# Performance work log

Hardware: AMD Instinct MI355X
Metric: run time of the kernel (lower is better)

Reference implementation:

```python
import jax, jax.numpy as jnp
import numpy as np

NUM_EMBEDDINGS = 1024
EMBEDDING_DIM = 256


def setup_inputs() -> dict:
    key = jax.random.key(0)
    k1, k2 = jax.random.split(key)
    x = jax.random.normal(k1, (64, EMBEDDING_DIM, 32, 32), dtype=jnp.float32)
    # torch.nn.init.uniform_ default is U[0,1)
    embeddings = jax.random.uniform(k2, (EMBEDDING_DIM, NUM_EMBEDDINGS), dtype=jnp.float32)
    return {"x": x, "embeddings": embeddings}


def reference(x, embeddings):
    # x: [B, C, H, W] with C == embedding_dim; embeddings: [D, K]
    B, C, H, W = x.shape
    x_perm = jnp.transpose(x, (0, 2, 3, 1))           # [B, H, W, D]
    flat = x_perm.reshape(-1, C)                      # [N, D]
    sim = flat @ embeddings                           # [N, K] GEMM
    dists = (jnp.sum(flat * flat, axis=1, keepdims=True)
             + jnp.sum(embeddings * embeddings, axis=0)
             - 2.0 * sim)                             # [N, K]
    indices = jnp.argmin(dists, axis=1)               # [N]
    # one-hot @ embeddings.T is just a row gather of embeddings.T
    quantized = embeddings.T[indices]                 # [N, D]
    quantized = quantized.reshape(x_perm.shape)       # [B, H, W, D]
    # straight-through estimator
    q_ste = x_perm + jax.lax.stop_gradient(quantized - x_perm)
    q_ste = jnp.transpose(q_ste, (0, 3, 1, 2))        # [B, C, H, W]
    quantized = jnp.transpose(quantized, (0, 3, 1, 2))
    return q_ste, quantized, indices
```

## Files before the change

kernel.cpp:

```cpp
#include <hip/hip_runtime.h>

typedef unsigned short u16;
typedef unsigned int   u32;

#define DCH  256
#define KCB  1024
#define HW   1024
#define NPOS 65536
#define MARGIN 0.12f

#define ESQ_WS   0
#define IDX_WS   4096
#define FCNT_WS  266240
#define FLIST_WS 266304
#define ESQD_WS  528448ull
#define XH_WS    1048576ull
#define EH_WS    34603008ull

using f32x4 = __attribute__((ext_vector_type(4))) float;
using f16x8 = __attribute__((ext_vector_type(8))) _Float16;

__device__ __forceinline__ u16 f2h(float x) {
    _Float16 h = (_Float16)x;
    return *reinterpret_cast<u16*>(&h);
}

__device__ __forceinline__ void gl_lds16(const void* g, void* l) {
    __builtin_amdgcn_global_load_lds(
        (const __attribute__((address_space(1))) void*)g,
        (__attribute__((address_space(3))) void*)l, 16, 0, 0);
}

__global__ __launch_bounds__(256) void prep_x(const float* __restrict__ src,
                                              u16* __restrict__ dst,
                                              int* __restrict__ fcnt) {
    __shared__ float Xs[32][260];
    const int tid = threadIdx.x;
    if (blockIdx.x == 0 && tid == 0) *fcnt = 0;
    const int b  = blockIdx.x >> 5;
    const int pc = (blockIdx.x >> 3) & 3;
    const int cc = blockIdx.x & 7;
    const int p0 = pc * 256;
    const int c0 = cc * 32;
    const size_t nbase = (size_t)b * 1024 + p0;

#pragma unroll
    for (int r = 0; r < 8; ++r) {
        int id4 = tid + 256 * r;
        int c = id4 >> 6;
        int q = id4 & 63;
        float4 v = *reinterpret_cast<const float4*>(
            src + (size_t)b * 262144 + (size_t)(c0 + c) * 1024 + p0 + q * 4);
        *reinterpret_cast<float4*>(&Xs[c][q * 4]) = v;
    }
    __syncthreads();

    const int p = tid;
#pragma unroll
    for (int dg = 0; dg < 4; ++dg) {
        u32 w0, w1, w2, w3;
        {
            float f0 = Xs[dg * 8 + 0][p], f1 = Xs[dg * 8 + 1][p];
            float f2 = Xs[dg * 8 + 2][p], f3 = Xs[dg * 8 + 3][p];
            float f4 = Xs[dg * 8 + 4][p], f5 = Xs[dg * 8 + 5][p];
            float f6 = Xs[dg * 8 + 6][p], f7 = Xs[dg * 8 + 7][p];
            w0 = (u32)f2h(f0) | ((u32)f2h(f1) << 16);
            w1 = (u32)f2h(f2) | ((u32)f2h(f3) << 16);
            w2 = (u32)f2h(f4) | ((u32)f2h(f5) << 16);
            w3 = (u32)f2h(f6) | ((u32)f2h(f7) << 16);
        }
        uint4 ov = {w0, w1, w2, w3};
        *reinterpret_cast<uint4*>(dst + (nbase + p) * 256 + c0 + dg * 8) = ov;
    }
}

__global__ __launch_bounds__(256) void esq_kernel(const float* __restrict__ E,
                                                  float* __restrict__ esq,
                                                  double* __restrict__ esqd) {
    int k = blockIdx.x * 256 + threadIdx.x;
    double s = 0.0;
#pragma unroll 8
    for (int c = 0; c < DCH; ++c) {
        double e = (double)E[c * KCB + k];
        s = fma(e, e, s);
    }
    esq[k] = (float)s;
    esqd[k] = s;
}

#define BUFS  16384
#define EH_O  8192
#define ESQ_O 32768
#define MRG_O 36864
#define SM_SZ 39936

__global__ __launch_bounds__(256, 2) void vq_main_mfma(
        const u16* __restrict__ XhG, const u16* __restrict__ EhG,
        const float* __restrict__ esq,
        int* __restrict__ idx_out, int* __restrict__ flag_cnt,
        int* __restrict__ flag_list) {
    __shared__ alignas(16) char sm[SM_SZ];
    const int tid = threadIdx.x;
    const int l = tid & 63;
    const int w = tid >> 6;
    const int wm = w >> 1, wn = w & 1;
    const int pbase = blockIdx.x * 128;

    *reinterpret_cast<float4*>(sm + ESQ_O + tid * 16) =
        *reinterpret_cast<const float4*>(esq + tid * 4);

    const int rowt0 = w * 32 + (l >> 2);
    const int slog = (l & 3) ^ ((rowt0 >> 1) & 3);
    const char* XhB = reinterpret_cast<const char*>(XhG);
    const char* EhB = reinterpret_cast<const char*>(EhG);
    const size_t xoff0 = (size_t)(pbase + rowt0) * 512 + slog * 16;
    const size_t eoff0 = (size_t)rowt0 * 512 + slog * 16;
    const int w2k = (w * 2) * 1024;

    const int rA = wm * 64 + (l & 15);
    const int addrA = rA * 64 + (((l >> 4) ^ ((rA >> 1) & 3)) * 16);
    const int rB = wn * 64 + (l & 15);
    const int addrB = rB * 64 + (((l >> 4) ^ ((rB >> 1) & 3)) * 16);

    auto STAGE = [&](int bufo, int nt, int dt) {
        size_t xo = xoff0 + (size_t)dt * 64;
        gl_lds16(XhB + xo,        sm + bufo + w2k);
        gl_lds16(XhB + xo + 8192, sm + bufo + w2k + 1024);
        size_t eo = eoff0 + (size_t)nt * 65536 + (size_t)dt * 64;
        gl_lds16(EhB + eo,        sm + bufo + EH_O + w2k);
        gl_lds16(EhB + eo + 8192, sm + bufo + EH_O + w2k + 1024);
    };

    float b1[16], b2[16];
    int   i1[16];
#pragma unroll
    for (int q = 0; q < 16; ++q) { b1[q] = 3.4e38f; b2[q] = 3.4e38f; i1[q] = 0; }

    STAGE(0, 0, 0);
    __syncthreads();

    int step = 0;
    for (int nt = 0; nt < 8; ++nt) {
        f32x4 acc[4][4];
#pragma unroll
        for (int i = 0; i < 4; ++i)
#pragma unroll
            for (int j = 0; j < 4; ++j)
#pragma unroll
                for (int r = 0; r < 4; ++r) acc[i][j][r] = 0.f;

        for (int dt = 0; dt < 8; ++dt) {
            int nxt = step + 1;
            if (nxt < 64) STAGE((nxt & 1) * BUFS, nxt >> 3, nxt & 7);
            const char* bo = sm + (step & 1) * BUFS;
            f16x8 a[4], bh[4];
#pragma unroll
            for (int i = 0; i < 4; ++i)
                a[i] = *reinterpret_cast<const f16x8*>(bo + addrA + i * 1024);
#pragma unroll
            for (int j = 0; j < 4; ++j)
                bh[j] = *reinterpret_cast<const f16x8*>(bo + EH_O + addrB + j * 1024);
#pragma unroll
            for (int i = 0; i < 4; ++i)
#pragma unroll
                for (int j = 0; j < 4; ++j)
                    acc[i][j] = __builtin_amdgcn_mfma_f32_16x16x32_f16(a[i], bh[j], acc[i][j], 0, 0, 0);
            __syncthreads();
            ++step;
        }

        const int kb = nt * 128 + wn * 64 + (l & 15);
        float eq[4];
#pragma unroll
        for (int j = 0; j < 4; ++j)
            eq[j] = *reinterpret_cast<const float*>(sm + ESQ_O + (kb + j * 16) * 4);
#pragma unroll
        for (int i = 0; i < 4; ++i)
#pragma unroll
            for (int j = 0; j < 4; ++j)
#pragma unroll
                for (int r = 0; r < 4; ++r) {
                    float s = fmaf(-2.f, acc[i][j][r], eq[j]);
                    int ri = i * 4 + r;
                    bool lt = s < b1[ri];
                    b2[ri] = fminf(b2[ri], fmaxf(s, b1[ri]));
                    i1[ri] = lt ? (kb + j * 16) : i1[ri];
                    b1[ri] = fminf(b1[ri], s);
                }
    }

#pragma unroll
    for (int m = 1; m <= 8; m <<= 1) {
#pragma unroll
        for (int q = 0; q < 16; ++q) {
            float ob1 = __shfl_xor(b1[q], m);
            float ob2 = __shfl_xor(b2[q], m);
            int   oi  = __shfl_xor(i1[q], m);
            bool lt = ob1 < b1[q];
            b2[q] = fminf(fminf(b2[q], ob2), fmaxf(b1[q], ob1));
            i1[q] = lt ? oi : i1[q];
            b1[q] = fminf(b1[q], ob1);
        }
    }

    if ((l & 15) == 0) {
#pragma unroll
        for (int i = 0; i < 4; ++i)
#pragma unroll
            for (int r = 0; r < 4; ++r) {
                int q = i * 4 + r;
                int rl = wm * 64 + i * 16 + (l >> 4) * 4 + r;
                *reinterpret_cast<float*>(sm + MRG_O + (rl * 2 + wn) * 4) = b1[q];
                *reinterpret_cast<float*>(sm + MRG_O + 1024 + (rl * 2 + wn) * 4) = b2[q];
                *reinterpret_cast<int*>(sm + MRG_O + 2048 + (rl * 2 + wn) * 4) = i1[q];
            }
    }
    __syncthreads();
    if (tid < 128) {
        float a1 = *reinterpret_cast<float*>(sm + MRG_O + (tid * 2 + 0) * 4);
        float a2 = *reinterpret_cast<float*>(sm + MRG_O + 1024 + (tid * 2 + 0) * 4);
        int   ai = *reinterpret_cast<int*>(sm + MRG_O + 2048 + (tid * 2 + 0) * 4);
        float c1 = *reinterpret_cast<float*>(sm + MRG_O + (tid * 2 + 1) * 4);
        float c2 = *reinterpret_cast<float*>(sm + MRG_O + 1024 + (tid * 2 + 1) * 4);
        int   ci = *reinterpret_cast<int*>(sm + MRG_O + 2048 + (tid * 2 + 1) * 4);
        bool lt = c1 < a1;
        float B1 = fminf(a1, c1);
        float B2 = fminf(fminf(a2, c2), fmaxf(a1, c1));
        int I1 = lt ? ci : ai;
        int n = pbase + tid;
        idx_out[n] = I1;
        if (B2 - B1 < MARGIN) {
            int s2 = atomicAdd(flag_cnt, 1);
            flag_list[s2] = n;
        }
    }
}

#define RFPB 4
__global__ __launch_bounds__(256) void vq_repair(const float* __restrict__ X,
                                                 const float* __restrict__ E,
                                                 const double* __restrict__ esqd,
                                                 int* __restrict__ idx_out,
                                                 const int* __restrict__ flag_cnt,
                                                 const int* __restrict__ flag_list) {
    __shared__ double xs[RFPB][256];
    __shared__ double rd[RFPB][256];
    __shared__ int    ri[RFPB][256];
    const int tid = threadIdx.x;
    const int cnt = *flag_cnt;
    for (int f0 = blockIdx.x * RFPB; f0 < cnt; f0 += gridDim.x * RFPB) {
#pragma unroll
        for (int g = 0; g < RFPB; ++g) {
            int f = f0 + g;
            int n = flag_list[f < cnt ? f : f0];
            int b = n >> 10, p = n & 1023;
            xs[g][tid] = (double)X[(size_t)b * 262144 + (size_t)tid * 1024 + p];
        }
        __syncthreads();
        double s[RFPB][4];
#pragma unroll
        for (int g = 0; g < RFPB; ++g)
#pragma unroll
            for (int j = 0; j < 4; ++j) s[g][j] = 0.0;
        const float4* Erow = reinterpret_cast<const float4*>(E) + tid;
#pragma unroll 2
        for (int c = 0; c < 256; ++c) {
            float4 ev = Erow[c * 256];
            double e0 = (double)ev.x, e1 = (double)ev.y, e2 = (double)ev.z, e3 = (double)ev.w;
#pragma unroll
            for (int g = 0; g < RFPB; ++g) {
                double xv = xs[g][c];
                s[g][0] = fma(xv, e0, s[g][0]);
                s[g][1] = fma(xv, e1, s[g][1]);
                s[g][2] = fma(xv, e2, s[g][2]);
                s[g][3] = fma(xv, e3, s[g][3]);
            }
        }
        const int k0 = tid * 4;
        const double eq0 = esqd[k0], eq1 = esqd[k0 + 1], eq2 = esqd[k0 + 2], eq3 = esqd[k0 + 3];
#pragma unroll
        for (int g = 0; g < RFPB; ++g) {
            double d0 = eq0 - 2.0 * s[g][0];
            double d1 = eq1 - 2.0 * s[g][1];
            double d2 = eq2 - 2.0 * s[g][2];
            double d3 = eq3 - 2.0 * s[g][3];
            double bd = d0; int bi = k0;
            if (d1 < bd) { bd = d1; bi = k0 + 1; }
            if (d2 < bd) { bd = d2; bi = k0 + 2; }
            if (d3 < bd) { bd = d3; bi = k0 + 3; }
            rd[g][tid] = bd; ri[g][tid] = bi;
        }
        __syncthreads();
        for (int off = 128; off > 0; off >>= 1) {
            if (tid < off) {
#pragma unroll
                for (int g = 0; g < RFPB; ++g) {
                    double od = rd[g][tid + off]; int oi = ri[g][tid + off];
                    if (od < rd[g][tid] || (od == rd[g][tid] && oi < ri[g][tid])) {
                        rd[g][tid] = od; ri[g][tid] = oi;
                    }
                }
            }
            __syncthreads();
        }
        if (tid < RFPB && (f0 + tid) < cnt) {
            idx_out[flag_list[f0 + tid]] = ri[tid][0];
        }
        __syncthreads();
    }
}

#define WCC 8
__global__ __launch_bounds__(256) void vq_write(const float* __restrict__ E,
                                                const int* __restrict__ idx_ws,
                                                float* __restrict__ out0,
                                                float* __restrict__ out1,
                                                float* __restrict__ out2) {
    __shared__ float Es[WCC][1024];
    const int tid = threadIdx.x;
    const int b   = blockIdx.x >> 5;
    const int cch = blockIdx.x & 31;
#pragma unroll
    for (int r = 0; r < 8; ++r) {
        int id4 = tid + 256 * r;
        int c = id4 >> 8;
        int q = id4 & 255;
        *reinterpret_cast<float4*>(&Es[c][q * 4]) =
            *reinterpret_cast<const float4*>(E + (size_t)(cch * WCC + c) * 1024 + q * 4);
    }
    int4 kv = *reinterpret_cast<const int4*>(idx_ws + b * 1024 + tid * 4);
    __syncthreads();
    if (cch == 0) {
        float4 v = {(float)kv.x, (float)kv.y, (float)kv.z, (float)kv.w};
        *reinterpret_cast<float4*>(out2 + b * 1024 + tid * 4) = v;
    }
#pragma unroll
    for (int c = 0; c < WCC; ++c) {
        float4 v = {Es[c][kv.x], Es[c][kv.y], Es[c][kv.z], Es[c][kv.w]};
        size_t o = (size_t)b * 262144 + (size_t)(cch * WCC + c) * 1024 + tid * 4;
        *reinterpret_cast<float4*>(out0 + o) = v;
        *reinterpret_cast<float4*>(out1 + o) = v;
    }
}

extern "C" void kernel_launch(void* const* d_in, const int* in_sizes, int n_in,
                              void* d_out, int out_size, void* d_ws, size_t ws_size,
                              hipStream_t stream) {
    const float* X = (const float*)d_in[0];
    const float* E = (const float*)d_in[1];
    float* out = (float*)d_out;
    char* ws = (char*)d_ws;

    float* esq   = (float*)(ws + ESQ_WS);
    int* idx     = (int*)(ws + IDX_WS);
    int* fcnt    = (int*)(ws + FCNT_WS);
    int* flist   = (int*)(ws + FLIST_WS);
    double* esqd = (double*)(ws + ESQD_WS);
    u16* Xh      = (u16*)(ws + XH_WS);
    u16* Eh      = (u16*)(ws + EH_WS);

    prep_x<<<2048, 256, 0, stream>>>(X, Xh, fcnt);
    prep_x<<<32, 256, 0, stream>>>(E, Eh, fcnt);
    esq_kernel<<<4, 256, 0, stream>>>(E, esq, esqd);
    vq_main_mfma<<<512, 256, 0, stream>>>(Xh, Eh, esq, idx, fcnt, flist);
    vq_repair<<<1024, 256, 0, stream>>>(X, E, esqd, idx, fcnt, flist);
    vq_write<<<2048, 256, 0, stream>>>(E, idx,
                                       out,
                                       out + 16777216,
                                       out + 33554432);
}
```

Baseline: 172.8 us.

## Fuse prep kernels, widen codebook tile, pack distance+index into u32 argmin

Merges the X transpose, E transpose and codebook-norm kernels into one launch. The main MFMA kernel now covers 256 codes per tile instead of 128, which halves the number of outer tiles and raises reuse of the X fragments. The argmin tracking packs a truncated nonnegative distance with the 10-bit code index into one u32, so best and second-best need only integer min/max and fewer shuffles. The repair margin is lowered from 0.12 to 0.10, so fewer positions go to the double-precision repair; the risk is that the truncated distances combined with the smaller margin miss some near ties.

```diff
diff --git a/kernel.cpp b/kernel.cpp
--- a/kernel.cpp
+++ b/kernel.cpp
@@ -7,7 +7,7 @@
 #define KCB  1024
 #define HW   1024
 #define NPOS 65536
-#define MARGIN 0.12f
+#define MARGIN 0.10f
 
 #define ESQ_WS   0
 #define IDX_WS   4096
@@ -24,6 +24,8 @@
     _Float16 h = (_Float16)x;
     return *reinterpret_cast<u16*>(&h);
 }
+__device__ __forceinline__ u32 umin2(u32 a, u32 b) { return a < b ? a : b; }
+__device__ __forceinline__ u32 umax2(u32 a, u32 b) { return a > b ? a : b; }
 
 __device__ __forceinline__ void gl_lds16(const void* g, void* l) {
     __builtin_amdgcn_global_load_lds(
@@ -31,19 +33,13 @@
         (__attribute__((address_space(3))) void*)l, 16, 0, 0);
 }
 
-__global__ __launch_bounds__(256) void prep_x(const float* __restrict__ src,
-                                              u16* __restrict__ dst,
-                                              int* __restrict__ fcnt) {
+__device__ __forceinline__ void transpose_slice(const float* __restrict__ src,
+                                                u16* __restrict__ dst,
+                                                int b, int pc, int cc, int tid) {
     __shared__ float Xs[32][260];
-    const int tid = threadIdx.x;
-    if (blockIdx.x == 0 && tid == 0) *fcnt = 0;
-    const int b  = blockIdx.x >> 5;
-    const int pc = (blockIdx.x >> 3) & 3;
-    const int cc = blockIdx.x & 7;
     const int p0 = pc * 256;
     const int c0 = cc * 32;
     const size_t nbase = (size_t)b * 1024 + p0;
-
 #pragma unroll
     for (int r = 0; r < 8; ++r) {
         int id4 = tid + 256 * r;
@@ -54,7 +50,6 @@
         *reinterpret_cast<float4*>(&Xs[c][q * 4]) = v;
     }
     __syncthreads();
-
     const int p = tid;
 #pragma unroll
     for (int dg = 0; dg < 4; ++dg) {
@@ -74,27 +69,41 @@
     }
 }
 
-__global__ __launch_bounds__(256) void esq_kernel(const float* __restrict__ E,
-                                                  float* __restrict__ esq,
-                                                  double* __restrict__ esqd) {
-    int k = blockIdx.x * 256 + threadIdx.x;
-    double s = 0.0;
+__global__ __launch_bounds__(256) void prep_all(const float* __restrict__ X,
+                                                const float* __restrict__ E,
+                                                u16* __restrict__ Xh,
+                                                u16* __restrict__ Eh,
+                                                float* __restrict__ esq,
+                                                double* __restrict__ esqd,
+                                                int* __restrict__ fcnt) {
+    const int tid = threadIdx.x;
+    const int bid = blockIdx.x;
+    if (bid < 2048) {
+        transpose_slice(X, Xh, bid >> 5, (bid >> 3) & 3, bid & 7, tid);
+    } else if (bid < 2080) {
+        int b2 = bid - 2048;
+        transpose_slice(E, Eh, 0, (b2 >> 3) & 3, b2 & 7, tid);
+    } else {
+        if (bid == 2080 && tid == 0) *fcnt = 0;
+        int k = (bid - 2080) * 256 + tid;
+        double s = 0.0;
 #pragma unroll 8
-    for (int c = 0; c < DCH; ++c) {
-        double e = (double)E[c * KCB + k];
-        s = fma(e, e, s);
-    }
-    esq[k] = (float)s;
-    esqd[k] = s;
-}
-
-#define BUFS  16384
-#define EH_O  8192
-#define ESQ_O 32768
-#define MRG_O 36864
-#define SM_SZ 39936
-
-__global__ __launch_bounds__(256, 2) void vq_main_mfma(
+        for (int c = 0; c < DCH; ++c) {
+            double e = (double)E[c * KCB + k];
+            s = fma(e, e, s);
+        }
+        esq[k] = (float)s;
+        esqd[k] = s;
+    }
+}
+
+#define BUFS  24576
+#define EB_O  8192
+#define ESQ_O 49152
+#define MRG_O 53248
+#define SM_SZ 55296
+
+__global__ __launch_bounds__(256, 2) void vq_main_mfma2(
         const u16* __restrict__ XhG, const u16* __restrict__ EhG,
         const float* __restrict__ esq,
         int* __restrict__ idx_out, int* __restrict__ flag_cnt,
@@ -109,83 +118,85 @@
     *reinterpret_cast<float4*>(sm + ESQ_O + tid * 16) =
         *reinterpret_cast<const float4*>(esq + tid * 4);
 
-    const int rowt0 = w * 32 + (l >> 2);
-    const int slog = (l & 3) ^ ((rowt0 >> 1) & 3);
+    const int rxt0 = w * 32 + (l >> 2);
+    const int slogx = (l & 3) ^ ((rxt0 >> 1) & 3);
+    const int ret0 = w * 64 + (l >> 2);
+    const int sloge = (l & 3) ^ ((ret0 >> 1) & 3);
     const char* XhB = reinterpret_cast<const char*>(XhG);
     const char* EhB = reinterpret_cast<const char*>(EhG);
-    const size_t xoff0 = (size_t)(pbase + rowt0) * 512 + slog * 16;
-    const size_t eoff0 = (size_t)rowt0 * 512 + slog * 16;
-    const int w2k = (w * 2) * 1024;
+    const size_t xoff0 = (size_t)(pbase + rxt0) * 512 + slogx * 16;
+    const size_t eoff0 = (size_t)ret0 * 512 + sloge * 16;
 
     const int rA = wm * 64 + (l & 15);
     const int addrA = rA * 64 + (((l >> 4) ^ ((rA >> 1) & 3)) * 16);
-    const int rB = wn * 64 + (l & 15);
+    const int rB = wn * 128 + (l & 15);
     const int addrB = rB * 64 + (((l >> 4) ^ ((rB >> 1) & 3)) * 16);
 
     auto STAGE = [&](int bufo, int nt, int dt) {
         size_t xo = xoff0 + (size_t)dt * 64;
-        gl_lds16(XhB + xo,        sm + bufo + w2k);
-        gl_lds16(XhB + xo + 8192, sm + bufo + w2k + 1024);
-        size_t eo = eoff0 + (size_t)nt * 65536 + (size_t)dt * 64;
-        gl_lds16(EhB + eo,        sm + bufo + EH_O + w2k);
-        gl_lds16(EhB + eo + 8192, sm + bufo + EH_O + w2k + 1024);
+        gl_lds16(XhB + xo,        sm + bufo + w * 2048);
+        gl_lds16(XhB + xo + 8192, sm + bufo + w * 2048 + 1024);
+        size_t eo = eoff0 + (size_t)nt * 131072 + (size_t)dt * 64;
+        gl_lds16(EhB + eo,         sm + bufo + EB_O + w * 4096);
+        gl_lds16(EhB + eo + 8192,  sm + bufo + EB_O + w * 4096 + 1024);
+        gl_lds16(EhB + eo + 16384, sm + bufo + EB_O + w * 4096 + 2048);
+        gl_lds16(EhB + eo + 24576, sm + bufo + EB_O + w * 4096 + 3072);
     };
 
-    float b1[16], b2[16];
-    int   i1[16];
-#pragma unroll
-    for (int q = 0; q < 16; ++q) { b1[q] = 3.4e38f; b2[q] = 3.4e38f; i1[q] = 0; }
+    u32 b1[16], b2[16];
+#pragma unroll
+    for (int q = 0; q < 16; ++q) { b1[q] = 0xFFFFFFFFu; b2[q] = 0xFFFFFFFFu; }
 
     STAGE(0, 0, 0);
     __syncthreads();
 
     int step = 0;
-    for (int nt = 0; nt < 8; ++nt) {
-        f32x4 acc[4][4];
+    for (int nt = 0; nt < 4; ++nt) {
+        f32x4 acc[4][8];
 #pragma unroll
         for (int i = 0; i < 4; ++i)
 #pragma unroll
-            for (int j = 0; j < 4; ++j)
+            for (int j = 0; j < 8; ++j)
 #pragma unroll
                 for (int r = 0; r < 4; ++r) acc[i][j][r] = 0.f;
 
         for (int dt = 0; dt < 8; ++dt) {
             int nxt = step + 1;
-            if (nxt < 64) STAGE((nxt & 1) * BUFS, nxt >> 3, nxt & 7);
+            if (nxt < 32) STAGE((nxt & 1) * BUFS, nxt >> 3, nxt & 7);
             const char* bo = sm + (step & 1) * BUFS;
-            f16x8 a[4], bh[4];
+            f16x8 a[4], bh[8];
 #pragma unroll
             for (int i = 0; i < 4; ++i)
                 a[i] = *reinterpret_cast<const f16x8*>(bo + addrA + i * 1024);
 #pragma unroll
-            for (int j = 0; j < 4; ++j)
-                bh[j] = *reinterpret_cast<const f16x8*>(bo + EH_O + addrB + j * 1024);
+            for (int j = 0; j < 8; ++j)
+                bh[j] = *reinterpret_cast<const f16x8*>(bo + EB_O + addrB + j * 1024);
 #pragma unroll
             for (int i = 0; i < 4; ++i)
 #pragma unroll
-                for (int j = 0; j < 4; ++j)
+                for (int j = 0; j < 8; ++j)
                     acc[i][j] = __builtin_amdgcn_mfma_f32_16x16x32_f16(a[i], bh[j], acc[i][j], 0, 0, 0);
             __syncthreads();
             ++step;
         }
 
-        const int kb = nt * 128 + wn * 64 + (l & 15);
-        float eq[4];
-#pragma unroll
-        for (int j = 0; j < 4; ++j)
+        const int kb = nt * 256 + wn * 128 + (l & 15);
+        float eq[8];
+#pragma unroll
+        for (int j = 0; j < 8; ++j)
             eq[j] = *reinterpret_cast<const float*>(sm + ESQ_O + (kb + j * 16) * 4);
 #pragma unroll
         for (int i = 0; i < 4; ++i)
 #pragma unroll
-            for (int j = 0; j < 4; ++j)
+            for (int j = 0; j < 8; ++j)
 #pragma unroll
                 for (int r = 0; r < 4; ++r) {
-                    float s = fmaf(-2.f, acc[i][j][r], eq[j]);
+                    float s = fmaxf(fmaf(-2.f, acc[i][j][r], eq[j]), 0.f);
+                    u32 v = (__float_as_uint(s) & 0xFFFFFC00u) | (u32)(kb + j * 16);
                     int ri = i * 4 + r;
-                    bool lt = s < b1[ri];
-                    b2[ri] = fminf(b2[ri], fmaxf(s, b1[ri]));
-                    i1[ri] = lt ? (kb + j * 16) : i1[ri];
-                    b1[ri] = fminf(b1[ri], s);
+                    u32 m1 = umin2(b1[ri], v);
+                    b2[ri] = umin2(b2[ri], umax2(b1[ri], v));
+                    b1[ri] = m1;
                 }
     }
 
@@ -193,13 +204,11 @@
     for (int m = 1; m <= 8; m <<= 1) {
 #pragma unroll
         for (int q = 0; q < 16; ++q) {
-            float ob1 = __shfl_xor(b1[q], m);
-            float ob2 = __shfl_xor(b2[q], m);
-            int   oi  = __shfl_xor(i1[q], m);
-            bool lt = ob1 < b1[q];
-            b2[q] = fminf(fminf(b2[q], ob2), fmaxf(b1[q], ob1));
-            i1[q] = lt ? oi : i1[q];
-            b1[q] = fminf(b1[q], ob1);
+            u32 ob1 = (u32)__shfl_xor((int)b1[q], m);
+            u32 ob2 = (u32)__shfl_xor((int)b2[q], m);
+            u32 mx = umax2(b1[q], ob1);
+            b1[q] = umin2(b1[q], ob1);
+            b2[q] = umin2(umin2(b2[q], ob2), mx);
         }
     }
 
@@ -210,26 +219,23 @@
             for (int r = 0; r < 4; ++r) {
                 int q = i * 4 + r;
                 int rl = wm * 64 + i * 16 + (l >> 4) * 4 + r;
-                *reinterpret_cast<float*>(sm + MRG_O + (rl * 2 + wn) * 4) = b1[q];
-                *reinterpret_cast<float*>(sm + MRG_O + 1024 + (rl * 2 + wn) * 4) = b2[q];
-                *reinterpret_cast<int*>(sm + MRG_O + 2048 + (rl * 2 + wn) * 4) = i1[q];
+                *reinterpret_cast<u32*>(sm + MRG_O + (rl * 2 + wn) * 4) = b1[q];
+                *reinterpret_cast<u32*>(sm + MRG_O + 1024 + (rl * 2 + wn) * 4) = b2[q];
             }
     }
     __syncthreads();
     if (tid < 128) {
-        float a1 = *reinterpret_cast<float*>(sm + MRG_O + (tid * 2 + 0) * 4);
-        float a2 = *reinterpret_cast<float*>(sm + MRG_O + 1024 + (tid * 2 + 0) * 4);
-        int   ai = *reinterpret_cast<int*>(sm + MRG_O + 2048 + (tid * 2 + 0) * 4);
-        float c1 = *reinterpret_cast<float*>(sm + MRG_O + (tid * 2 + 1) * 4);
-        float c2 = *reinterpret_cast<float*>(sm + MRG_O + 1024 + (tid * 2 + 1) * 4);
-        int   ci = *reinterpret_cast<int*>(sm + MRG_O + 2048 + (tid * 2 + 1) * 4);
-        bool lt = c1 < a1;
-        float B1 = fminf(a1, c1);
-        float B2 = fminf(fminf(a2, c2), fmaxf(a1, c1));
-        int I1 = lt ? ci : ai;
+        u32 a1 = *reinterpret_cast<u32*>(sm + MRG_O + (tid * 2 + 0) * 4);
+        u32 a2 = *reinterpret_cast<u32*>(sm + MRG_O + 1024 + (tid * 2 + 0) * 4);
+        u32 c1 = *reinterpret_cast<u32*>(sm + MRG_O + (tid * 2 + 1) * 4);
+        u32 c2 = *reinterpret_cast<u32*>(sm + MRG_O + 1024 + (tid * 2 + 1) * 4);
+        u32 P1 = umin2(a1, c1);
+        u32 P2 = umin2(umin2(a2, c2), umax2(a1, c1));
         int n = pbase + tid;
-        idx_out[n] = I1;
-        if (B2 - B1 < MARGIN) {
+        idx_out[n] = (int)(P1 & 1023u);
+        float f1 = __uint_as_float(P1 & 0xFFFFFC00u);
+        float f2 = __uint_as_float(P2 & 0xFFFFFC00u);
+        if (f2 - f1 < MARGIN) {
             int s2 = atomicAdd(flag_cnt, 1);
             flag_list[s2] = n;
         }
@@ -359,10 +365,8 @@
     u16* Xh      = (u16*)(ws + XH_WS);
     u16* Eh      = (u16*)(ws + EH_WS);
 
-    prep_x<<<2048, 256, 0, stream>>>(X, Xh, fcnt);
-    prep_x<<<32, 256, 0, stream>>>(E, Eh, fcnt);
-    esq_kernel<<<4, 256, 0, stream>>>(E, esq, esqd);
-    vq_main_mfma<<<512, 256, 0, stream>>>(Xh, Eh, esq, idx, fcnt, flist);
+    prep_all<<<2084, 256, 0, stream>>>(X, E, Xh, Eh, esq, esqd, fcnt);
+    vq_main_mfma2<<<512, 256, 0, stream>>>(Xh, Eh, esq, idx, fcnt, flist);
     vq_repair<<<1024, 256, 0, stream>>>(X, E, esqd, idx, fcnt, flist);
     vq_write<<<2048, 256, 0, stream>>>(E, idx,
                                        out,
```

New measurement: 201.8 us. 16.8% more time.
